# Kernel tuning notes

Hardware: AMD Instinct MI355X
Metric: run time of the kernel (lower is better)

## Reference

```python
import jax, jax.numpy as jnp
import numpy as np

B, LQ, H, NH, LK, N = 32, 256, 256, 8, 512, 8192
DH = H // NH
EPS = 1e-12

def layer_norm(x, g, b):
    m = x.mean(-1, keepdims=True)
    v = ((x - m) ** 2).mean(-1, keepdims=True)
    return (x - m) / jnp.sqrt(v + EPS) * g + b

def setup_inputs() -> dict:
    rs = np.random.RandomState(0)
    counts = rs.randint(LK // 2, LK + 1, size=B)  # ragged per-graph edge counts, max = LK
    E = int(counts.sum())
    edge_batch = jnp.asarray(np.repeat(np.arange(B), counts), jnp.int32)
    edge_pos = jnp.asarray(np.concatenate([np.arange(c) for c in counts]), jnp.int32)
    pad_mask = jnp.asarray((np.arange(LK)[None, :] < counts[:, None]).astype(np.float32))
    src = jnp.asarray(rs.randint(0, N, E), jnp.int32)
    dst = jnp.asarray(rs.randint(0, N, E), jnp.int32)
    ks = jax.random.split(jax.random.key(0), 16)
    def rn(i, shape, s=0.02):
        return jax.random.normal(ks[i], shape, jnp.float32) * s
    return dict(
        extended_attention_mask=jnp.zeros((B, 1, 1, LQ), jnp.float32),
        query=rn(0, (B, LQ, H), 1.0),
        rel_embedding_output=rn(1, (E, H), 1.0),
        graph_output=rn(2, (N, H), 1.0),
        src=src, dst=dst, edge_batch=edge_batch, edge_pos=edge_pos, pad_mask=pad_mask,
        Wq=rn(3, (H, H)), bq=jnp.zeros((H,), jnp.float32),
        Wk=rn(4, (2 * H, H)), bk=jnp.zeros((H,), jnp.float32),
        Wv=rn(5, (H, H)), bv=jnp.zeros((H,), jnp.float32),
        Wo=rn(6, (H, H)), bo=jnp.zeros((H,), jnp.float32),
        ln1_g=jnp.ones((H,), jnp.float32), ln1_b=jnp.zeros((H,), jnp.float32),
        W1=rn(7, (H, H)), b1=jnp.zeros((H,), jnp.float32),
        W2=rn(8, (H, H)), b2=jnp.zeros((H,), jnp.float32),
        ln2_g=jnp.ones((H,), jnp.float32), ln2_b=jnp.zeros((H,), jnp.float32),
    )

def reference(extended_attention_mask, query, rel_embedding_output, graph_output,
              src, dst, edge_batch, edge_pos, pad_mask,
              Wq, bq, Wk, bk, Wv, bv, Wo, bo, ln1_g, ln1_b,
              W1, b1, W2, b2, ln2_g, ln2_b):
    # --- memory_transform: edge gather + ragged pad (vectorized scatter) ---
    key_flat = jnp.concatenate([graph_output[src], rel_embedding_output], -1)  # [E, 2H]
    dst_flat = graph_output[dst]                                               # [E, H]
    key_pad = jnp.zeros((B, LK, 2 * H), key_flat.dtype).at[edge_batch, edge_pos].set(key_flat)
    val_pad = jnp.zeros((B, LK, H), dst_flat.dtype).at[edge_batch, edge_pos].set(dst_flat)
    cross_mask = (1.0 - pad_mask)[:, None, None, :] * -10000.0                 # [B,1,1,LK]
    # --- BidiAttention ---
    Q = (query @ Wq + bq).reshape(B, LQ, NH, DH)
    K = (key_pad @ Wk + bk).reshape(B, LK, NH, DH)
    V = (val_pad @ Wv + bv).reshape(B, LK, NH, DH)
    scores = jnp.einsum('bqhd,bkhd->bhqk', Q, K) / np.float32(np.sqrt(DH))
    pq = jax.nn.softmax(scores + cross_mask, axis=-1)
    query_ctx = jnp.einsum('bhqk,bkhd->bqhd', pq, V).reshape(B, LQ, H)
    pv = jax.nn.softmax(scores.transpose(0, 1, 3, 2) + extended_attention_mask, axis=-1)
    value_ctx = jnp.einsum('bhkq,bqhd->bkhd', pv, Q).reshape(B, LK, H)
    # --- RelAwareCross output / gate ---
    query_out = layer_norm(query_ctx @ Wo + bo + query, ln1_g, ln1_b)
    theta = jax.nn.sigmoid(value_ctx @ W1 + b1 + val_pad @ W2 + b2)
    value_new = layer_norm(theta * value_ctx + (1.0 - theta) * val_pad, ln2_g, ln2_b)
    # --- memory_update: unpad + scatter-mean by dst, replace rows with incoming edges ---
    val_edges = value_new[edge_batch, edge_pos]                                # [E, H]
    sums = jax.ops.segment_sum(val_edges, dst, num_segments=N)
    cnts = jax.ops.segment_sum(jnp.ones((val_edges.shape[0],), val_edges.dtype), dst, num_segments=N)
    mean = sums / jnp.maximum(cnts, 1.0)[:, None]
    graph_new = jnp.where((cnts > 0)[:, None], mean, graph_output)
    return (graph_new, query_out)
```

## Files before the change

kernel.cpp:

```cpp
#include <hip/hip_runtime.h>
#include <hip/hip_bf16.h>
#include <string.h>

#define B_ 32
#define LQ_ 256
#define H_ 256
#define NH_ 8
#define LK_ 512
#define N_ 8192
#define DH_ 32

typedef float floatx4 __attribute__((ext_vector_type(4)));
typedef short shortx8 __attribute__((ext_vector_type(8)));
typedef short shortx4 __attribute__((ext_vector_type(4)));

__device__ __forceinline__ short f2b(float f) {
    __hip_bfloat16 h = __float2bfloat16(f);
    short s;
    __builtin_memcpy(&s, &h, 2);
    return s;
}
__device__ __forceinline__ float b2f(short s) {
    unsigned u = ((unsigned)(unsigned short)s) << 16;
    float f;
    __builtin_memcpy(&f, &u, 4);
    return f;
}

#define LOG2E 1.44269504088896f

__global__ __launch_bounds__(256) void phase1(
    const float* __restrict__ graph, const float* __restrict__ rel,
    const int* __restrict__ src, const int* __restrict__ dst,
    const int* __restrict__ eb, const float* __restrict__ pad_mask,
    const float* __restrict__ Wq, const float* __restrict__ Wk,
    const float* __restrict__ Wv, const float* __restrict__ Wo,
    const float* __restrict__ W1, const float* __restrict__ W2,
    short* __restrict__ WT, short* __restrict__ key_pad,
    short* __restrict__ val_pad, float* __restrict__ zbase, int E) {
    const int bid = blockIdx.x, tid = threadIdx.x;
    if (bid < 8192) {
        int row = bid * 2 + (tid >> 7);
        int t = tid & 127;
        int b = row >> 9, p = row & 511;
        bool valid = pad_mask[row] > 0.5f;
        size_t krow = (size_t)row * 512;
        size_t vrow = (size_t)row * 256;
        int kc = t * 4, vc = t * 2;
        if (valid) {
            int lo = 0, hi = E;
            while (lo < hi) { int mid = (lo + hi) >> 1; if (eb[mid] < b) lo = mid + 1; else hi = mid; }
            int e = lo + p;
            int s = src[e], d = dst[e];
            const float* sp = (kc < 256) ? (graph + (size_t)s * 256 + kc)
                                         : (rel + (size_t)e * 256 + (kc - 256));
            float4 k4 = *(const float4*)sp;
            key_pad[krow + kc + 0] = f2b(k4.x);
            key_pad[krow + kc + 1] = f2b(k4.y);
            key_pad[krow + kc + 2] = f2b(k4.z);
            key_pad[krow + kc + 3] = f2b(k4.w);
            float2 v2 = *(const float2*)(graph + (size_t)d * 256 + vc);
            val_pad[vrow + vc + 0] = f2b(v2.x);
            val_pad[vrow + vc + 1] = f2b(v2.y);
        } else {
            *(long long*)&key_pad[krow + kc] = 0;
            *(int*)&val_pad[vrow + vc] = 0;
        }
    } else if (bid < 9984) {
        int i = (bid - 8192) * 256 + tid;
        const float* s;
        int K, loc;
        if (i < 65536) { s = Wq; K = 256; loc = i; }
        else if (i < 196608) { s = Wk; K = 512; loc = i - 65536; }
        else {
            int m = (i - 196608) >> 16;
            loc = (i - 196608) & 65535;
            K = 256;
            s = (m == 0) ? Wv : (m == 1) ? Wo : (m == 2) ? W1 : W2;
        }
        int n = loc / K, k = loc - n * K;
        WT[i] = f2b(s[(size_t)k * 256 + n]);
    } else {
        long long n = (long long)N_ * H_ + N_;
        for (long long i = (long long)(bid - 9984) * 256 + tid; i < n; i += 512 * 256)
            zbase[i] = 0.f;
    }
}

__global__ __launch_bounds__(256) void phase2_gemm(
    const float* __restrict__ query, const short* __restrict__ key_pad,
    const short* __restrict__ val_pad, const short* __restrict__ WT,
    const float* __restrict__ bq, const float* __restrict__ bk,
    const float* __restrict__ bv,
    short* __restrict__ Qb, short* __restrict__ Kb,
    short* __restrict__ Vt, short* __restrict__ Qt) {
    __shared__ short As[64][40];
    __shared__ short Bs[64][40];
    const int tid = threadIdx.x;
    const int id = blockIdx.x;
    const float* Af = nullptr; const short* Ab = nullptr;
    const float* Bf = nullptr; const short* Bb = nullptr;
    const float* bias; short* C;
    size_t cbase; int cstride, K; bool biasM;
    if (id < 512) {
        int rb = id >> 2, cb = id & 3;
        Af = query + (size_t)(rb * 64) * 256; K = 256;
        Bb = WT + (size_t)(cb * 64) * 256;
        bias = bq + cb * 64; biasM = false;
        C = Qb; cbase = (size_t)(rb * 64) * 256 + cb * 64; cstride = 256;
    } else if (id < 1536) {
        int t = id - 512; int rb = t >> 2, cb = t & 3;
        Ab = key_pad + (size_t)(rb * 64) * 512; K = 512;
        Bb = WT + 65536 + (size_t)(cb * 64) * 512;
        bias = bk + cb * 64; biasM = false;
        C = Kb; cbase = (size_t)(rb * 64) * 256 + cb * 64; cstride = 256;
    } else if (id < 2560) {
        int t = id - 1536; int b = t >> 5, ct = (t >> 3) & 3, kt = t & 7;
        Ab = WT + 196608 + (size_t)(ct * 64) * 256; K = 256;
        Bb = val_pad + ((size_t)(b * 512 + kt * 64)) * 256;
        bias = bv + ct * 64; biasM = true;
        C = Vt; cbase = ((size_t)(b * 256 + ct * 64)) * 512 + kt * 64; cstride = 512;
    } else {
        int t = id - 2560; int b = t >> 4, ct = (t >> 2) & 3, qt = t & 3;
        Ab = WT + (size_t)(ct * 64) * 256; K = 256;
        Bf = query + ((size_t)(b * 256 + qt * 64)) * 256;
        bias = bq + ct * 64; biasM = true;
        C = Qt; cbase = ((size_t)(b * 256 + ct * 64)) * 256 + qt * 64; cstride = 256;
    }
    const int wv = tid >> 6, lane = tid & 63;
    const int mw = (wv & 1) * 32, nw = (wv >> 1) * 32;
    const int lm = lane & 15, quad = lane >> 4;

    floatx4 acc[2][2] = {{{0.f, 0.f, 0.f, 0.f}, {0.f, 0.f, 0.f, 0.f}},
                         {{0.f, 0.f, 0.f, 0.f}, {0.f, 0.f, 0.f, 0.f}}};

    for (int kc = 0; kc < K; kc += 32) {
        int r = tid >> 2, kq = (tid & 3) * 8;
        if (Af) {
            const float* ap = Af + (size_t)r * K + kc + kq;
            float4 a1 = *(const float4*)ap, a2 = *(const float4*)(ap + 4);
            As[r][kq + 0] = f2b(a1.x); As[r][kq + 1] = f2b(a1.y);
            As[r][kq + 2] = f2b(a1.z); As[r][kq + 3] = f2b(a1.w);
            As[r][kq + 4] = f2b(a2.x); As[r][kq + 5] = f2b(a2.y);
            As[r][kq + 6] = f2b(a2.z); As[r][kq + 7] = f2b(a2.w);
        } else {
            *(shortx8*)&As[r][kq] = *(const shortx8*)(Ab + (size_t)r * K + kc + kq);
        }
        if (Bf) {
            const float* bp = Bf + (size_t)r * K + kc + kq;
            float4 b1 = *(const float4*)bp, b2 = *(const float4*)(bp + 4);
            Bs[r][kq + 0] = f2b(b1.x); Bs[r][kq + 1] = f2b(b1.y);
            Bs[r][kq + 2] = f2b(b1.z); Bs[r][kq + 3] = f2b(b1.w);
            Bs[r][kq + 4] = f2b(b2.x); Bs[r][kq + 5] = f2b(b2.y);
            Bs[r][kq + 6] = f2b(b2.z); Bs[r][kq + 7] = f2b(b2.w);
        } else {
            *(shortx8*)&Bs[r][kq] = *(const shortx8*)(Bb + (size_t)r * K + kc + kq);
        }
        __syncthreads();
        shortx8 a0 = *(const shortx8*)&As[mw + lm][quad * 8];
        shortx8 a1 = *(const shortx8*)&As[mw + 16 + lm][quad * 8];
        shortx8 b0 = *(const shortx8*)&Bs[nw + lm][quad * 8];
        shortx8 b1 = *(const shortx8*)&Bs[nw + 16 + lm][quad * 8];
        acc[0][0] = __builtin_amdgcn_mfma_f32_16x16x32_bf16(a0, b0, acc[0][0], 0, 0, 0);
        acc[0][1] = __builtin_amdgcn_mfma_f32_16x16x32_bf16(a0, b1, acc[0][1], 0, 0, 0);
        acc[1][0] = __builtin_amdgcn_mfma_f32_16x16x32_bf16(a1, b0, acc[1][0], 0, 0, 0);
        acc[1][1] = __builtin_amdgcn_mfma_f32_16x16x32_bf16(a1, b1, acc[1][1], 0, 0, 0);
        __syncthreads();
    }
#pragma unroll
    for (int i = 0; i < 2; i++) {
#pragma unroll
        for (int j = 0; j < 2; j++) {
            int gn = nw + j * 16 + lm;
#pragma unroll
            for (int r = 0; r < 4; r++) {
                int gm = mw + i * 16 + quad * 4 + r;
                float bvv = biasM ? bias[gm] : bias[gn];
                C[cbase + (size_t)gm * cstride + gn] = f2b(acc[i][j][r] + bvv);
            }
        }
    }
}

__global__ __launch_bounds__(512, 4) void phase3_attn(
    const short* __restrict__ Qm, const short* __restrict__ Km,
    const short* __restrict__ Vt, const short* __restrict__ Qt,
    const float* __restrict__ pad_mask, const float* __restrict__ ext,
    short* __restrict__ qctx, short* __restrict__ vctx) {
    __shared__ short SA[128][40];
    __shared__ short ST[32][136];
    __shared__ short P[8][32][72];
    const int tid = threadIdx.x;
    const int w = tid >> 6, lane = tid & 63;
    const int lm = lane & 15, quad = lane >> 4;
    const float scale2 = 0.17677669529663687f * LOG2E;
    const int id = blockIdx.x;
    short (*Pw)[72] = P[w];

    if (id < 256) {
        const int b = id >> 3, h = id & 7;
        shortx8 bqf[2];
        bqf[0] = *(const shortx8*)(Qm + ((size_t)(b * 256 + w * 32 + lm)) * 256 + h * 32 + quad * 8);
        bqf[1] = *(const shortx8*)(Qm + ((size_t)(b * 256 + w * 32 + 16 + lm)) * 256 + h * 32 + quad * 8);
        floatx4 oacc[2][2] = {{{0.f,0.f,0.f,0.f},{0.f,0.f,0.f,0.f}},
                              {{0.f,0.f,0.f,0.f},{0.f,0.f,0.f,0.f}}};
        float psum[2] = {0.f, 0.f};
        const floatx4* pmp = (const floatx4*)(pad_mask + b * 512);
        for (int kc = 0; kc < 512; kc += 128) {
            if (tid < 256) {
                int r = tid >> 1, dq = (tid & 1) * 16;
                const short* kp = Km + ((size_t)(b * 512 + kc + r)) * 256 + h * 32 + dq;
                *(shortx8*)&SA[r][dq] = *(const shortx8*)kp;
                *(shortx8*)&SA[r][dq + 8] = *(const shortx8*)(kp + 8);
            } else {
                int u = tid - 256;
                int r = u >> 3, kq = (u & 7) * 16;
                const short* vp = Vt + ((size_t)(b * 256 + h * 32 + r)) * 512 + kc + kq;
                *(shortx8*)&ST[r][kq] = *(const shortx8*)vp;
                *(shortx8*)&ST[r][kq + 8] = *(const shortx8*)(vp + 8);
            }
            __syncthreads();
#pragma unroll
            for (int kh = 0; kh < 2; kh++) {
#pragma unroll
                for (int kt = 0; kt < 4; kt++) {
                    shortx8 ak = *(const shortx8*)&SA[kh * 64 + kt * 16 + lm][quad * 8];
                    floatx4 pm = pmp[kc / 4 + kh * 16 + kt * 4 + quad];
#pragma unroll
                    for (int qf = 0; qf < 2; qf++) {
                        floatx4 s = {0.f, 0.f, 0.f, 0.f};
                        s = __builtin_amdgcn_mfma_f32_16x16x32_bf16(ak, bqf[qf], s, 0, 0, 0);
                        shortx4 p4;
#pragma unroll
                        for (int r = 0; r < 4; r++) {
                            float e = __builtin_amdgcn_exp2f(
                                s[r] * scale2 + (1.0f - pm[r]) * (-10000.0f * LOG2E));
                            psum[qf] += e;
                            p4[r] = f2b(e);
                        }
                        *(long long*)&Pw[qf * 16 + lm][kt * 16 + quad * 4] = *(long long*)&p4;
                    }
                }
#pragma unroll
                for (int ks = 0; ks < 2; ks++) {
#pragma unroll
                    for (int qf = 0; qf < 2; qf++) {
                        shortx8 pb = *(const shortx8*)&Pw[qf * 16 + lm][ks * 32 + quad * 8];
#pragma unroll
                        for (int di = 0; di < 2; di++) {
                            shortx8 av = *(const shortx8*)&ST[di * 16 + lm][kh * 64 + ks * 32 + quad * 8];
                            oacc[qf][di] = __builtin_amdgcn_mfma_f32_16x16x32_bf16(av, pb, oacc[qf][di], 0, 0, 0);
                        }
                    }
                }
            }
            __syncthreads();
        }
#pragma unroll
        for (int qf = 0; qf < 2; qf++) {
            psum[qf] += __shfl_xor(psum[qf], 16, 64);
            psum[qf] += __shfl_xor(psum[qf], 32, 64);
            float inv = 1.0f / psum[qf];
            int q = w * 32 + qf * 16 + lm;
            short* op = qctx + ((size_t)(b * 256 + q)) * 256 + h * 32;
#pragma unroll
            for (int di = 0; di < 2; di++) {
                shortx4 o;
#pragma unroll
                for (int r = 0; r < 4; r++) o[r] = f2b(oacc[qf][di][r] * inv);
                *(long long*)(op + di * 16 + quad * 4) = *(long long*)&o;
            }
        }
    } else {
        const int t = id - 256;
        const int b = t >> 4, h = (t >> 1) & 7, khb = t & 1;
        shortx8 bkf[2];
        bkf[0] = *(const shortx8*)(Km + ((size_t)(b * 512 + khb * 256 + w * 32 + lm)) * 256 + h * 32 + quad * 8);
        bkf[1] = *(const shortx8*)(Km + ((size_t)(b * 512 + khb * 256 + w * 32 + 16 + lm)) * 256 + h * 32 + quad * 8);
        floatx4 oacc[2][2] = {{{0.f,0.f,0.f,0.f},{0.f,0.f,0.f,0.f}},
                              {{0.f,0.f,0.f,0.f},{0.f,0.f,0.f,0.f}}};
        float psum[2] = {0.f, 0.f};
        const floatx4* emp = (const floatx4*)(ext + b * 256);
        for (int qc = 0; qc < 256; qc += 128) {
            if (tid < 256) {
                int r = tid >> 1, dq = (tid & 1) * 16;
                const short* qp = Qm + ((size_t)(b * 256 + qc + r)) * 256 + h * 32 + dq;
                *(shortx8*)&SA[r][dq] = *(const shortx8*)qp;
                *(shortx8*)&SA[r][dq + 8] = *(const shortx8*)(qp + 8);
            } else {
                int u = tid - 256;
                int r = u >> 3, kq = (u & 7) * 16;
                const short* tp = Qt + ((size_t)(b * 256 + h * 32 + r)) * 256 + qc + kq;
                *(shortx8*)&ST[r][kq] = *(const shortx8*)tp;
                *(shortx8*)&ST[r][kq + 8] = *(const shortx8*)(tp + 8);
            }
            __syncthreads();
#pragma unroll
            for (int qh = 0; qh < 2; qh++) {
#pragma unroll
                for (int qt = 0; qt < 4; qt++) {
                    shortx8 aq = *(const shortx8*)&SA[qh * 64 + qt * 16 + lm][quad * 8];
                    floatx4 em = emp[qc / 4 + qh * 16 + qt * 4 + quad];
#pragma unroll
                    for (int kf = 0; kf < 2; kf++) {
                        floatx4 s = {0.f, 0.f, 0.f, 0.f};
                        s = __builtin_amdgcn_mfma_f32_16x16x32_bf16(aq, bkf[kf], s, 0, 0, 0);
                        shortx4 p4;
#pragma unroll
                        for (int r = 0; r < 4; r++) {
                            float e = __builtin_amdgcn_exp2f(s[r] * scale2 + em[r] * LOG2E);
                            psum[kf] += e;
                            p4[r] = f2b(e);
                        }
                        *(long long*)&Pw[kf * 16 + lm][qt * 16 + quad * 4] = *(long long*)&p4;
                    }
                }
#pragma unroll
                for (int ks = 0; ks < 2; ks++) {
#pragma unroll
                    for (int kf = 0; kf < 2; kf++) {
                        shortx8 pb = *(const shortx8*)&Pw[kf * 16 + lm][ks * 32 + quad * 8];
#pragma unroll
                        for (int di = 0; di < 2; di++) {
                            shortx8 aT = *(const shortx8*)&ST[di * 16 + lm][qh * 64 + ks * 32 + quad * 8];
                            oacc[kf][di] = __builtin_amdgcn_mfma_f32_16x16x32_bf16(aT, pb, oacc[kf][di], 0, 0, 0);
                        }
                    }
                }
            }
            __syncthreads();
        }
#pragma unroll
        for (int kf = 0; kf < 2; kf++) {
            psum[kf] += __shfl_xor(psum[kf], 16, 64);
            psum[kf] += __shfl_xor(psum[kf], 32, 64);
            float inv = 1.0f / psum[kf];
            int k = khb * 256 + w * 32 + kf * 16 + lm;
            short* op = vctx + ((size_t)(b * 512 + k)) * 256 + h * 32;
#pragma unroll
            for (int di = 0; di < 2; di++) {
                shortx4 o;
#pragma unroll
                for (int r = 0; r < 4; r++) o[r] = f2b(oacc[kf][di][r] * inv);
                *(long long*)(op + di * 16 + quad * 4) = *(long long*)&o;
            }
        }
    }
}

__global__ __launch_bounds__(256) void phase4a_gemm(
    const short* __restrict__ qctx, const short* __restrict__ vctx,
    const short* __restrict__ val_pad, const short* __restrict__ WTo,
    const short* __restrict__ WT1, const short* __restrict__ WT2,
    float* __restrict__ obuf, float* __restrict__ tbuf) {
    __shared__ short As1[64][40];
    __shared__ short As2[64][40];
    __shared__ short Bs1[64][40];
    __shared__ short Bs2[64][40];
    const int tid = threadIdx.x;
    const int id = blockIdx.x;
    const bool is_out = id < 512;
    int t = is_out ? id : id - 512;
    const int row0 = (t >> 2) * 64, col0 = (t & 3) * 64;
    const int wv = tid >> 6, lane = tid & 63;
    const int mw = (wv & 1) * 32, nw = (wv >> 1) * 32;
    const int lm = lane & 15, quad = lane >> 4;

    floatx4 acc[2][2] = {{{0.f, 0.f, 0.f, 0.f}, {0.f, 0.f, 0.f, 0.f}},
                         {{0.f, 0.f, 0.f, 0.f}, {0.f, 0.f, 0.f, 0.f}}};

    for (int kc = 0; kc < 256; kc += 32) {
        int r = tid >> 2, kq = (tid & 3) * 8;
        if (is_out) {
            *(shortx8*)&As1[r][kq] =
                *(const shortx8*)(qctx + (size_t)(row0 + r) * 256 + kc + kq);
            *(shortx8*)&Bs1[r][kq] =
                *(const shortx8*)(WTo + (size_t)(col0 + r) * 256 + kc + kq);
        } else {
            *(shortx8*)&As1[r][kq] =
                *(const shortx8*)(vctx + (size_t)(row0 + r) * 256 + kc + kq);
            *(shortx8*)&As2[r][kq] =
                *(const shortx8*)(val_pad + (size_t)(row0 + r) * 256 + kc + kq);
            *(shortx8*)&Bs1[r][kq] =
                *(const shortx8*)(WT1 + (size_t)(col0 + r) * 256 + kc + kq);
            *(shortx8*)&Bs2[r][kq] =
                *(const shortx8*)(WT2 + (size_t)(col0 + r) * 256 + kc + kq);
        }
        __syncthreads();
        shortx8 a0 = *(const shortx8*)&As1[mw + lm][quad * 8];
        shortx8 a1 = *(const shortx8*)&As1[mw + 16 + lm][quad * 8];
        shortx8 b0 = *(const shortx8*)&Bs1[nw + lm][quad * 8];
        shortx8 b1 = *(const shortx8*)&Bs1[nw + 16 + lm][quad * 8];
        acc[0][0] = __builtin_amdgcn_mfma_f32_16x16x32_bf16(a0, b0, acc[0][0], 0, 0, 0);
        acc[0][1] = __builtin_amdgcn_mfma_f32_16x16x32_bf16(a0, b1, acc[0][1], 0, 0, 0);
        acc[1][0] = __builtin_amdgcn_mfma_f32_16x16x32_bf16(a1, b0, acc[1][0], 0, 0, 0);
        acc[1][1] = __builtin_amdgcn_mfma_f32_16x16x32_bf16(a1, b1, acc[1][1], 0, 0, 0);
        if (!is_out) {
            shortx8 c0 = *(const shortx8*)&As2[mw + lm][quad * 8];
            shortx8 c1 = *(const shortx8*)&As2[mw + 16 + lm][quad * 8];
            shortx8 d0 = *(const shortx8*)&Bs2[nw + lm][quad * 8];
            shortx8 d1 = *(const shortx8*)&Bs2[nw + 16 + lm][quad * 8];
            acc[0][0] = __builtin_amdgcn_mfma_f32_16x16x32_bf16(c0, d0, acc[0][0], 0, 0, 0);
            acc[0][1] = __builtin_amdgcn_mfma_f32_16x16x32_bf16(c0, d1, acc[0][1], 0, 0, 0);
            acc[1][0] = __builtin_amdgcn_mfma_f32_16x16x32_bf16(c1, d0, acc[1][0], 0, 0, 0);
            acc[1][1] = __builtin_amdgcn_mfma_f32_16x16x32_bf16(c1, d1, acc[1][1], 0, 0, 0);
        }
        __syncthreads();
    }
    float* C = is_out ? obuf : tbuf;
#pragma unroll
    for (int i = 0; i < 2; i++) {
#pragma unroll
        for (int j = 0; j < 2; j++) {
            int gn = col0 + nw + j * 16 + lm;
#pragma unroll
            for (int r = 0; r < 4; r++) {
                int gm = row0 + mw + i * 16 + quad * 4 + r;
                C[(size_t)gm * 256 + gn] = acc[i][j][r];
            }
        }
    }
}

__global__ __launch_bounds__(256) void phase4b_ln(
    const float* __restrict__ obuf, const float* __restrict__ bo,
    const float* __restrict__ query, const float* __restrict__ g1,
    const float* __restrict__ be1, float* __restrict__ out_q,
    const float* __restrict__ tbuf, const short* __restrict__ vctx,
    const short* __restrict__ val_pad, const float* __restrict__ b1_,
    const float* __restrict__ b2_, const float* __restrict__ g2,
    const float* __restrict__ be2, const float* __restrict__ pad_mask,
    const int* __restrict__ eb, const int* __restrict__ dst,
    float* __restrict__ sums, int* __restrict__ icnts, int E) {
    const int lane = threadIdx.x & 63, w = threadIdx.x >> 6;
    const int c0 = lane * 4;
    if (blockIdx.x < 2048) {
        int row = blockIdx.x * 4 + w;
        long long base = (long long)row * H_ + c0;
        float4 o = *(const float4*)(obuf + base);
        float4 bo4 = *(const float4*)(bo + c0);
        float4 q4 = *(const float4*)(query + base);
        float x0 = o.x + bo4.x + q4.x, x1 = o.y + bo4.y + q4.y;
        float x2 = o.z + bo4.z + q4.z, x3 = o.w + bo4.w + q4.w;
        float t = x0 + x1 + x2 + x3;
        for (int off = 32; off > 0; off >>= 1) t += __shfl_xor(t, off, 64);
        float mean = t * (1.0f / H_);
        float d0 = x0 - mean, d1 = x1 - mean, d2 = x2 - mean, d3 = x3 - mean;
        float v = d0 * d0 + d1 * d1 + d2 * d2 + d3 * d3;
        for (int off = 32; off > 0; off >>= 1) v += __shfl_xor(v, off, 64);
        float rs = rsqrtf(v * (1.0f / H_) + 1e-12f);
        float4 g = *(const float4*)(g1 + c0);
        float4 be = *(const float4*)(be1 + c0);
        float4 out;
        out.x = d0 * rs * g.x + be.x; out.y = d1 * rs * g.y + be.y;
        out.z = d2 * rs * g.z + be.z; out.w = d3 * rs * g.w + be.w;
        *(float4*)(out_q + base) = out;
    } else {
        int row = (blockIdx.x - 2048) * 4 + w;
        if (pad_mask[row] > 0.5f) {
            long long base = (long long)row * H_ + c0;
            float4 tb = *(const float4*)(tbuf + base);
            float4 b14 = *(const float4*)(b1_ + c0);
            float4 b24 = *(const float4*)(b2_ + c0);
            shortx4 vc = *(const shortx4*)(vctx + base);
            shortx4 vp = *(const shortx4*)(val_pad + base);
            float x[4];
#pragma unroll
            for (int j = 0; j < 4; j++) {
                float tv = (j == 0) ? tb.x : (j == 1) ? tb.y : (j == 2) ? tb.z : tb.w;
                float bb1 = (j == 0) ? b14.x : (j == 1) ? b14.y : (j == 2) ? b14.z : b14.w;
                float bb2 = (j == 0) ? b24.x : (j == 1) ? b24.y : (j == 2) ? b24.z : b24.w;
                float th = 1.0f / (1.0f + __expf(-(tv + bb1 + bb2)));
                x[j] = th * b2f(vc[j]) + (1.0f - th) * b2f(vp[j]);
            }
            float t = x[0] + x[1] + x[2] + x[3];
            for (int off = 32; off > 0; off >>= 1) t += __shfl_xor(t, off, 64);
            float mean = t * (1.0f / H_);
            float d0 = x[0] - mean, d1 = x[1] - mean, d2 = x[2] - mean, d3 = x[3] - mean;
            float v = d0 * d0 + d1 * d1 + d2 * d2 + d3 * d3;
            for (int off = 32; off > 0; off >>= 1) v += __shfl_xor(v, off, 64);
            float rs = rsqrtf(v * (1.0f / H_) + 1e-12f);
            float4 g = *(const float4*)(g2 + c0);
            float4 be = *(const float4*)(be2 + c0);
            float y0 = d0 * rs * g.x + be.x, y1 = d1 * rs * g.y + be.y;
            float y2 = d2 * rs * g.z + be.z, y3 = d3 * rs * g.w + be.w;
            int b = row >> 9;
            int lo = 0, hi = E;
            while (lo < hi) { int mid = (lo + hi) >> 1; if (eb[mid] < b) lo = mid + 1; else hi = mid; }
            int d = dst[lo + (row & 511)];
            float* sp = sums + (size_t)d * 256 + c0;
            atomicAdd(sp + 0, y0);
            atomicAdd(sp + 1, y1);
            atomicAdd(sp + 2, y2);
            atomicAdd(sp + 3, y3);
            if (lane == 0) atomicAdd(&icnts[d], 1);
        }
    }
}

__global__ __launch_bounds__(256) void finalize_graph(
    const float* __restrict__ sums, const int* __restrict__ icnts,
    const float* __restrict__ graph, float* __restrict__ out_g) {
    int n = blockIdx.x, c = threadIdx.x;
    long long idx = (long long)n * H_ + c;
    int cnt = icnts[n];
    out_g[idx] = (cnt > 0) ? sums[idx] / (float)cnt : graph[idx];
}

extern "C" void kernel_launch(void* const* d_in, const int* in_sizes, int n_in,
                              void* d_out, int out_size, void* d_ws, size_t ws_size,
                              hipStream_t stream) {
    const float* ext_mask = (const float*)d_in[0];
    const float* query    = (const float*)d_in[1];
    const float* rel      = (const float*)d_in[2];
    const float* graph    = (const float*)d_in[3];
    const int*  src      = (const int*)d_in[4];
    const int*  dst      = (const int*)d_in[5];
    const int*  eb       = (const int*)d_in[6];
    const int*  ep       = (const int*)d_in[7];
    const float* pad_mask = (const float*)d_in[8];
    const float* Wq = (const float*)d_in[9];  const float* bq = (const float*)d_in[10];
    const float* Wk = (const float*)d_in[11]; const float* bk = (const float*)d_in[12];
    const float* Wv = (const float*)d_in[13]; const float* bv = (const float*)d_in[14];
    const float* Wo = (const float*)d_in[15]; const float* bo = (const float*)d_in[16];
    const float* g1 = (const float*)d_in[17]; const float* be1 = (const float*)d_in[18];
    const float* W1 = (const float*)d_in[19]; const float* b1 = (const float*)d_in[20];
    const float* W2 = (const float*)d_in[21]; const float* b2 = (const float*)d_in[22];
    const float* g2 = (const float*)d_in[23]; const float* be2 = (const float*)d_in[24];
    const int E = in_sizes[2] / H_;
    (void)ep;

    float* out_g = (float*)d_out;
    float* out_q = (float*)d_out + (size_t)N_ * H_;

    short* sp = (short*)d_ws;
    short* key_pad = sp; sp += (size_t)B_ * LK_ * 2 * H_;
    short* val_pad = sp; sp += (size_t)B_ * LK_ * H_;
    short* Qb      = sp; sp += (size_t)B_ * LQ_ * H_;
    short* Kb      = sp; sp += (size_t)B_ * LK_ * H_;
    short* Vt      = sp; sp += (size_t)B_ * H_ * LK_;
    short* Qt      = sp; sp += (size_t)B_ * H_ * LQ_;
    short* qctx    = sp; sp += (size_t)B_ * LQ_ * H_;
    short* vctx    = sp; sp += (size_t)B_ * LK_ * H_;
    short* WT      = sp; sp += 458752;
    short* WTo = WT + 262144;
    short* WT1 = WT + 327680;
    short* WT2 = WT + 393216;
    float* fp = (float*)(((size_t)sp + 15) & ~(size_t)15);
    float* sums = fp; fp += (size_t)N_ * H_;
    int*   icnts = (int*)fp; fp += N_;
    float* obuf = fp; fp += (size_t)B_ * LQ_ * H_;
    float* tbuf = fp; fp += (size_t)B_ * LK_ * H_;

    phase1<<<10496, 256, 0, stream>>>(graph, rel, src, dst, eb, pad_mask,
                                      Wq, Wk, Wv, Wo, W1, W2,
                                      WT, key_pad, val_pad, sums, E);
    phase2_gemm<<<3072, 256, 0, stream>>>(query, key_pad, val_pad, WT,
                                          bq, bk, bv, Qb, Kb, Vt, Qt);
    phase3_attn<<<768, 512, 0, stream>>>(Qb, Kb, Vt, Qt, pad_mask, ext_mask,
                                         qctx, vctx);
    phase4a_gemm<<<1536, 256, 0, stream>>>(qctx, vctx, val_pad, WTo, WT1, WT2,
                                           obuf, tbuf);
    phase4b_ln<<<6144, 256, 0, stream>>>(obuf, bo, query, g1, be1, out_q,
                                         tbuf, vctx, val_pad, b1, b2, g2, be2,
                                         pad_mask, eb, dst, sums, icnts, E);
    finalize_graph<<<N_, 256, 0, stream>>>(sums, icnts, graph, out_g);
}
```

Before: 282.7 us.

## Replace atomic scatter-mean with per-node linked lists gathered in finalize

```diff
diff --git a/kernel.cpp b/kernel.cpp
--- a/kernel.cpp
+++ b/kernel.cpp
@@ -32,12 +32,14 @@
 __global__ __launch_bounds__(256) void phase1(
     const float* __restrict__ graph, const float* __restrict__ rel,
     const int* __restrict__ src, const int* __restrict__ dst,
-    const int* __restrict__ eb, const float* __restrict__ pad_mask,
+    const int* __restrict__ eb, const int* __restrict__ ep,
+    const float* __restrict__ pad_mask,
     const float* __restrict__ Wq, const float* __restrict__ Wk,
     const float* __restrict__ Wv, const float* __restrict__ Wo,
     const float* __restrict__ W1, const float* __restrict__ W2,
     short* __restrict__ WT, short* __restrict__ key_pad,
-    short* __restrict__ val_pad, float* __restrict__ zbase, int E) {
+    short* __restrict__ val_pad, int* __restrict__ head,
+    int* __restrict__ row2e, int E) {
     const int bid = blockIdx.x, tid = threadIdx.x;
     if (bid < 8192) {
         int row = bid * 2 + (tid >> 7);
@@ -81,9 +83,10 @@
         int n = loc / K, k = loc - n * K;
         WT[i] = f2b(s[(size_t)k * 256 + n]);
     } else {
-        long long n = (long long)N_ * H_ + N_;
-        for (long long i = (long long)(bid - 9984) * 256 + tid; i < n; i += 512 * 256)
-            zbase[i] = 0.f;
+        int i = (bid - 9984) * 256 + tid;
+        if (i < 8192) head[i] = -1;
+        for (int j = i; j < E; j += 8192)
+            row2e[eb[j] * 512 + ep[j]] = j;
     }
 }
 
@@ -426,12 +429,12 @@
     const float* __restrict__ obuf, const float* __restrict__ bo,
     const float* __restrict__ query, const float* __restrict__ g1,
     const float* __restrict__ be1, float* __restrict__ out_q,
-    const float* __restrict__ tbuf, const short* __restrict__ vctx,
+    float* __restrict__ tbuf, const short* __restrict__ vctx,
     const short* __restrict__ val_pad, const float* __restrict__ b1_,
     const float* __restrict__ b2_, const float* __restrict__ g2,
     const float* __restrict__ be2, const float* __restrict__ pad_mask,
-    const int* __restrict__ eb, const int* __restrict__ dst,
-    float* __restrict__ sums, int* __restrict__ icnts, int E) {
+    const int* __restrict__ row2e, const int* __restrict__ dst,
+    int* __restrict__ head, int* __restrict__ nxt) {
     const int lane = threadIdx.x & 63, w = threadIdx.x >> 6;
     const int c0 = lane * 4;
     if (blockIdx.x < 2048) {
@@ -482,29 +485,35 @@
             float rs = rsqrtf(v * (1.0f / H_) + 1e-12f);
             float4 g = *(const float4*)(g2 + c0);
             float4 be = *(const float4*)(be2 + c0);
-            float y0 = d0 * rs * g.x + be.x, y1 = d1 * rs * g.y + be.y;
-            float y2 = d2 * rs * g.z + be.z, y3 = d3 * rs * g.w + be.w;
-            int b = row >> 9;
-            int lo = 0, hi = E;
-            while (lo < hi) { int mid = (lo + hi) >> 1; if (eb[mid] < b) lo = mid + 1; else hi = mid; }
-            int d = dst[lo + (row & 511)];
-            float* sp = sums + (size_t)d * 256 + c0;
-            atomicAdd(sp + 0, y0);
-            atomicAdd(sp + 1, y1);
-            atomicAdd(sp + 2, y2);
-            atomicAdd(sp + 3, y3);
-            if (lane == 0) atomicAdd(&icnts[d], 1);
+            float4 y4;
+            y4.x = d0 * rs * g.x + be.x; y4.y = d1 * rs * g.y + be.y;
+            y4.z = d2 * rs * g.z + be.z; y4.w = d3 * rs * g.w + be.w;
+            *(float4*)(tbuf + base) = y4;
+            if (lane == 0) {
+                int d = dst[row2e[row]];
+                int prev = atomicExch(&head[d], row);
+                nxt[row] = prev;
+            }
         }
     }
 }
 
 __global__ __launch_bounds__(256) void finalize_graph(
-    const float* __restrict__ sums, const int* __restrict__ icnts,
-    const float* __restrict__ graph, float* __restrict__ out_g) {
+    const int* __restrict__ head, const int* __restrict__ nxt,
+    const float* __restrict__ yrows, const float* __restrict__ graph,
+    float* __restrict__ out_g) {
     int n = blockIdx.x, c = threadIdx.x;
     long long idx = (long long)n * H_ + c;
-    int cnt = icnts[n];
-    out_g[idx] = (cnt > 0) ? sums[idx] / (float)cnt : graph[idx];
+    int e = head[n];
+    if (e < 0) { out_g[idx] = graph[idx]; return; }
+    float acc = 0.f;
+    int cnt = 0;
+    while (e >= 0) {
+        acc += yrows[(size_t)e * H_ + c];
+        cnt++;
+        e = nxt[e];
+    }
+    out_g[idx] = acc / (float)cnt;
 }
 
 extern "C" void kernel_launch(void* const* d_in, const int* in_sizes, int n_in,
@@ -528,7 +537,6 @@
     const float* W2 = (const float*)d_in[21]; const float* b2 = (const float*)d_in[22];
     const float* g2 = (const float*)d_in[23]; const float* be2 = (const float*)d_in[24];
     const int E = in_sizes[2] / H_;
-    (void)ep;
 
     float* out_g = (float*)d_out;
     float* out_q = (float*)d_out + (size_t)N_ * H_;
@@ -546,15 +554,17 @@
     short* WTo = WT + 262144;
     short* WT1 = WT + 327680;
     short* WT2 = WT + 393216;
-    float* fp = (float*)(((size_t)sp + 15) & ~(size_t)15);
-    float* sums = fp; fp += (size_t)N_ * H_;
-    int*   icnts = (int*)fp; fp += N_;
+    int* ip = (int*)(((size_t)sp + 15) & ~(size_t)15);
+    int* head  = ip; ip += N_;
+    int* nxt   = ip; ip += B_ * LK_;
+    int* row2e = ip; ip += B_ * LK_;
+    float* fp = (float*)ip;
     float* obuf = fp; fp += (size_t)B_ * LQ_ * H_;
     float* tbuf = fp; fp += (size_t)B_ * LK_ * H_;
 
-    phase1<<<10496, 256, 0, stream>>>(graph, rel, src, dst, eb, pad_mask,
+    phase1<<<10016, 256, 0, stream>>>(graph, rel, src, dst, eb, ep, pad_mask,
                                       Wq, Wk, Wv, Wo, W1, W2,
-                                      WT, key_pad, val_pad, sums, E);
+                                      WT, key_pad, val_pad, head, row2e, E);
     phase2_gemm<<<3072, 256, 0, stream>>>(query, key_pad, val_pad, WT,
                                           bq, bk, bv, Qb, Kb, Vt, Qt);
     phase3_attn<<<768, 512, 0, stream>>>(Qb, Kb, Vt, Qt, pad_mask, ext_mask,
@@ -563,6 +573,6 @@
                                            obuf, tbuf);
     phase4b_ln<<<6144, 256, 0, stream>>>(obuf, bo, query, g1, be1, out_q,
                                          tbuf, vctx, val_pad, b1, b2, g2, be2,
-                                         pad_mask, eb, dst, sums, icnts, E);
-    finalize_graph<<<N_, 256, 0, stream>>>(sums, icnts, graph, out_g);
-}
+                                         pad_mask, row2e, dst, head, nxt);
+    finalize_graph<<<N_, 256, 0, stream>>>(head, nxt, tbuf, graph, out_g);
+}
```

Result: faster. 245.1 us (-13.3%).
